# Optimization experiments

Hardware: AMD Instinct MI355X
Metric: run time of the kernel (lower is better)

## Reference

```python
import jax, jax.numpy as jnp
import numpy as np

S = 4          # num species networks (H,C,N,O)
E = 8          # ensemble size
D = 384        # AEV dim
H1, H2, H3 = 160, 128, 96
N_ATOMS = 40000
ALPHA = 0.1    # CELU alpha used by torchani


def _celu(x):
    return jax.nn.celu(x, alpha=ALPHA)


def setup_inputs() -> dict:
    key = jax.random.key(0)
    ks = jax.random.split(key, 12)
    species = jax.random.randint(ks[0], (1, N_ATOMS), 0, S, dtype=jnp.int64)
    aev = jax.random.normal(ks[1], (1, N_ATOMS, D), dtype=jnp.float32)
    def w(k, shape, fan_in):
        return jax.random.normal(k, shape, dtype=jnp.float32) * (1.0 / np.sqrt(fan_in))
    W1 = w(ks[2], (S, E, D, H1), D)
    b1 = jnp.zeros((S, E, 1, H1), jnp.float32)
    W2 = w(ks[3], (S, E, H1, H2), H1)
    b2 = jnp.zeros((S, E, 1, H2), jnp.float32)
    W3 = w(ks[4], (S, E, H2, H3), H2)
    b3 = jnp.zeros((S, E, 1, H3), jnp.float32)
    W4 = w(ks[5], (S, E, H3, 1), H3)
    b4 = jnp.zeros((S, E, 1, 1), jnp.float32)
    return {"species": species, "aev": aev,
            "W1": W1, "b1": b1, "W2": W2, "b2": b2,
            "W3": W3, "b3": b3, "W4": W4, "b4": b4}


def reference(species, aev, W1, b1, W2, b2, W3, b3, W4, b4):
    sp = species.reshape(-1)                  # [N]
    x = aev.reshape(-1, aev.shape[-1])        # [N, D]
    # BmmNetwork per species: expand input over ensemble, baddbmm + CELU layers
    h = _celu(jnp.einsum('nd,sedo->seno', x, W1) + b1)     # [S,E,N,H1]
    h = _celu(jnp.einsum('send,sedo->seno', h, W2) + b2)   # [S,E,N,H2]
    h = _celu(jnp.einsum('send,sedo->seno', h, W3) + b3)   # [S,E,N,H3]
    h = jnp.einsum('send,sedo->seno', h, W4) + b4          # [S,E,N,1]
    per_atom = h.mean(axis=1)[..., 0]                      # [S,N] ensemble mean
    # select each atom's own species network output (gather/scatter of original)
    atom_e = per_atom[sp, jnp.arange(sp.shape[0])]         # [N]
    energy = jnp.sum(atom_e).reshape(1, 1)
    return energy
```

## Files before the change

kernel.cpp:

```cpp
#include <hip/hip_runtime.h>

typedef _Float16 half8 __attribute__((ext_vector_type(8)));
typedef float f32x16 __attribute__((ext_vector_type(16)));

#define NATOMS 40000
#define D_AEV  384

constexpr int S_NUM = 4, E_NUM = 8;
constexpr int H1W = 160, H2W = 128, H3W = 96;
constexpr float ALPHA = 0.1f;
constexpr int HBLK = (NATOMS + 255) / 256;
constexpr int TMAX = NATOMS / 128 + S_NUM + 1;
constexpr int GRID = 2 * TMAX;

constexpr size_t OFF_CNT    = 0;
constexpr size_t OFF_BC     = 256;
constexpr size_t OFF_BOFF   = OFF_BC + (size_t)HBLK * S_NUM * 4;
constexpr size_t OFF_BUCKET = (OFF_BOFF + (size_t)HBLK * S_NUM * 4 + 255) & ~(size_t)255;
constexpr size_t OFF_PART   = OFF_BUCKET + (size_t)S_NUM * NATOMS * 4;
constexpr size_t OFF_WT1    = (OFF_PART + (size_t)GRID * 4 + 255) & ~(size_t)255;
constexpr size_t OFF_WT2    = OFF_WT1 + (size_t)S_NUM * E_NUM * H1W * D_AEV * 2;
constexpr size_t OFF_WT3    = OFF_WT2 + (size_t)S_NUM * E_NUM * H2W * H1W * 2;


__device__ __forceinline__ void gload_lds16(const _Float16* g, _Float16* l) {
    __builtin_amdgcn_global_load_lds((const __attribute__((address_space(1))) void*)g,
                                     (__attribute__((address_space(3))) void*)l, 16, 0, 0);
}

#define VMW(n) asm volatile("s_waitcnt vmcnt(" #n ")" ::: "memory")
#define BARR() do { asm volatile("" ::: "memory"); __builtin_amdgcn_s_barrier(); \
                    asm volatile("" ::: "memory"); } while (0)

__device__ __forceinline__ float celu_f(float x) {
    return x > 0.f ? x : fmaf(ALPHA, __expf(x * (1.f / ALPHA)), -ALPHA);
}

__device__ __forceinline__ unsigned pk2(float a, float b) {
    auto p = __builtin_amdgcn_cvt_pkrtz(a, b);
    unsigned u; __builtin_memcpy(&u, &p, 4); return u;
}

template <int NL>
__device__ __forceinline__ void stage(const _Float16* we, const int* vo, int c0, _Float16* buf) {
#pragma unroll
    for (int it = 0; it < NL; ++it)
        gload_lds16(we + vo[it] + c0, buf + ((size_t)threadIdx.x + it * 256) * 8);
}

template <int OUTW, int KS16, int NFT>
__device__ __forceinline__ void consume32(const _Float16* buf, const half8* bf,
                                          f32x16* acc, int l31, int lhi) {
    __builtin_amdgcn_s_setprio(1);
#pragma unroll
    for (int t = 0; t < KS16; ++t) {
        half8 b = bf[t];
#pragma unroll
        for (int f = 0; f < NFT; ++f) {
            half8 a = *(const half8*)&buf[(((2 * t + lhi) * OUTW) + f * 32 + l31) * 8];
            acc[f] = __builtin_amdgcn_mfma_f32_32x32x16_f16(a, b, acc[f], 0, 0, 0);
        }
    }
    __builtin_amdgcn_s_setprio(0);
}

template <int NFT>
__device__ __forceinline__ void epilogue(const f32x16* acc, const float* LB, int boff,
                                         int lhi, half8* out) {
#pragma unroll
    for (int f = 0; f < NFT; ++f) {
        float val[16];
#pragma unroll
        for (int rb = 0; rb < 4; ++rb) {
            float4 bb = *(const float4*)&LB[boff + f * 32 + rb * 8 + lhi * 4];
#pragma unroll
            for (int j = 0; j < 4; ++j)
                val[rb * 4 + j] = celu_f(acc[f][rb * 4 + j] + ((const float*)&bb)[j]);
        }
        unsigned wrd[8], xw[8];
#pragma unroll
        for (int i = 0; i < 8; ++i) wrd[i] = pk2(val[2 * i], val[2 * i + 1]);
#pragma unroll
        for (int i = 0; i < 8; ++i) xw[i] = __shfl_xor(wrd[i], 32);
        unsigned f0[4], f1[4];
#pragma unroll
        for (int i = 0; i < 2; ++i) {
            f0[i]     = lhi ? xw[2 + i]  : wrd[i];
            f0[2 + i] = lhi ? wrd[2 + i] : xw[i];
            f1[i]     = lhi ? xw[6 + i]  : wrd[4 + i];
            f1[2 + i] = lhi ? wrd[6 + i] : xw[4 + i];
        }
        __builtin_memcpy(&out[2 * f], f0, 16);
        __builtin_memcpy(&out[2 * f + 1], f1, 16);
    }
}


__global__ void hist_kernel(const int* __restrict__ species, int* __restrict__ bc) {
    __shared__ int h[S_NUM];
    int t = threadIdx.x;
    if (t < S_NUM) h[t] = 0;
    __syncthreads();
    int i = blockIdx.x * 256 + t;
    if (i < NATOMS) atomicAdd(&h[species[i]], 1);
    __syncthreads();
    if (t < S_NUM) bc[blockIdx.x * S_NUM + t] = h[t];
}

__global__ void scan_kernel(const int* __restrict__ bc, int* __restrict__ boff,
                            int* __restrict__ counts) {
    int w = threadIdx.x >> 6;
    int l = threadIdx.x & 63;
    int run = 0;
    for (int r = 0; r < (HBLK + 63) / 64; ++r) {
        int b = r * 64 + l;
        int v = (b < HBLK) ? bc[b * S_NUM + w] : 0;
        int x = v;
#pragma unroll
        for (int d = 1; d < 64; d <<= 1) { int y = __shfl_up(x, d); if (l >= d) x += y; }
        if (b < HBLK) boff[b * S_NUM + w] = run + x - v;
        run += __shfl(x, 63);
    }
    if (l == 0) counts[w] = run;
}

__global__ void scatter_kernel(const int* __restrict__ species, const int* __restrict__ boff,
                               int* __restrict__ bucket) {
    __shared__ int h[S_NUM];
    int t = threadIdx.x;
    if (t < S_NUM) h[t] = 0;
    __syncthreads();
    int i = blockIdx.x * 256 + t;
    if (i < NATOMS) {
        int sp = species[i];
        int r = atomicAdd(&h[sp], 1);
        bucket[sp * NATOMS + boff[blockIdx.x * S_NUM + sp] + r] = i;
    }
}

__global__ void transpose_all(const float* __restrict__ W1, const float* __restrict__ W2,
                              const float* __restrict__ W3, _Float16* __restrict__ wt1,
                              _Float16* __restrict__ wt2, _Float16* __restrict__ wt3) {
    __shared__ float t[32][33];
    int z = blockIdx.z;
    int m = z & 31;
    const float* src; _Float16* dst; int R, C;
    if (z < 32)      { src = W1; dst = wt1; R = D_AEV; C = H1W; }
    else if (z < 64) { src = W2; dst = wt2; R = H1W;  C = H2W; }
    else             { src = W3; dst = wt3; R = H2W;  C = H3W; }
    int c0 = blockIdx.x * 32, r0 = blockIdx.y * 32;
    if (c0 >= C || r0 >= R) return;
    src += (size_t)m * R * C;
    dst += (size_t)m * R * C;
    int tx = threadIdx.x, ty = threadIdx.y;
#pragma unroll
    for (int j = 0; j < 32; j += 8)
        t[ty + j][tx] = src[(size_t)(r0 + ty + j) * C + c0 + tx];
    __syncthreads();
#pragma unroll
    for (int j = 0; j < 32; j += 8)
        dst[(size_t)(c0 + ty + j) * R + r0 + tx] = (_Float16)t[tx][ty + j];
}


__global__ void __launch_bounds__(256, 2)
mlp_main(const int* __restrict__ counts, const int* __restrict__ bucket,
         const float* __restrict__ aev,
         const _Float16* __restrict__ wt1, const _Float16* __restrict__ wt2,
         const _Float16* __restrict__ wt3,
         const float* __restrict__ b1, const float* __restrict__ b2,
         const float* __restrict__ b3,
         const float* __restrict__ w4,
         float* __restrict__ partials) {
    __shared__ __align__(16) _Float16 WB[3][8 * H1W * 8];
    __shared__ __align__(16) float Lbias[4 * 480];
    __shared__ float part[4];

    const int bid = blockIdx.x;
    const int eb = bid & 1;
    const int t = bid >> 1;
    const int tid = threadIdx.x;

    int cnt0 = counts[0], cnt1 = counts[1], cnt2 = counts[2], cnt3 = counts[3];
    int n0 = (cnt0 + 127) >> 7, n1 = (cnt1 + 127) >> 7, n2 = (cnt2 + 127) >> 7;
    int n3 = (cnt3 + 127) >> 7;
    int s, t0, cnt;
    if (t < n0)                { s = 0; t0 = t; cnt = cnt0; }
    else if (t < n0 + n1)      { s = 1; t0 = t - n0; cnt = cnt1; }
    else if (t < n0 + n1 + n2) { s = 2; t0 = t - n0 - n1; cnt = cnt2; }
    else if (t < n0 + n1 + n2 + n3) { s = 3; t0 = t - n0 - n1 - n2; cnt = cnt3; }
    else { if (tid == 0) partials[bid] = 0.f; return; }
    const int base = t0 * 128;

    const int l = tid & 63, w = tid >> 6;
    const int l31 = l & 31, lhi = l >> 5;
    _Float16* B0 = WB[0]; _Float16* B1 = WB[1]; _Float16* B2 = WB[2];

    for (int u = tid; u < 4 * 480; u += 256) {
        int el = u / 480, o = u % 480;
        int se = s * E_NUM + eb * 4 + el;
        float v;
        if (o < 160)      v = b1[se * H1W + o];
        else if (o < 288) v = b2[se * H2W + (o - 160)];
        else if (o < 384) v = b3[se * H3W + (o - 288)];
        else              v = w4[se * H3W + (o - 384)];
        Lbias[u] = v;
    }
    __syncthreads();

    int aidx = bucket[s * NATOMS + min(base + w * 32 + l31, cnt - 1)];
    const float* xr = aev + (size_t)aidx * D_AEV + lhi * 8;
    half8 xa[24];
#pragma unroll
    for (int kk = 0; kk < 24; ++kk) {
        float4 f0 = *(const float4*)(xr + kk * 16);
        float4 f1 = *(const float4*)(xr + kk * 16 + 4);
        half8 h;
        h[0] = (_Float16)f0.x; h[1] = (_Float16)f0.y; h[2] = (_Float16)f0.z; h[3] = (_Float16)f0.w;
        h[4] = (_Float16)f1.x; h[5] = (_Float16)f1.y; h[6] = (_Float16)f1.z; h[7] = (_Float16)f1.w;
        xa[kk] = h;
    }
    VMW(0);

    int vo1[5], vo2[4], vo3[3];
#pragma unroll
    for (int it = 0; it < 5; ++it) { int u = tid + it * 256; vo1[it] = (u % H1W) * D_AEV + (u / H1W) * 8; }
#pragma unroll
    for (int it = 0; it < 4; ++it) { int u = tid + it * 256; vo2[it] = (u & 127) * H1W + (u >> 7) * 8; }
#pragma unroll
    for (int it = 0; it < 3; ++it) { int u = tid + it * 256; vo3[it] = (u % H3W) * H2W + (u / H3W) * 8; }

    float eacc = 0.f;
    const int se0 = s * E_NUM + eb * 4;

    {
        const _Float16* w1e0 = wt1 + (size_t)se0 * (H1W * D_AEV);
        stage<5>(w1e0, vo1, 0, B0);
        stage<5>(w1e0, vo1, 64, B1);
    }

#pragma unroll 1
    for (int el = 0; el < 4; ++el) {
        const int se = se0 + el;
        const _Float16* w1e = wt1 + (size_t)se * (H1W * D_AEV);
        const _Float16* w2e = wt2 + (size_t)se * (H2W * H1W);
        const _Float16* w3e = wt3 + (size_t)se * (H3W * H2W);
        const _Float16* w1n = wt1 + (size_t)(se + (el < 3 ? 1 : 0)) * (H1W * D_AEV);
        const float* LB = Lbias + el * 480;

        f32x16 c1a[5], c2a[4], c3a[3];
#pragma unroll
        for (int f = 0; f < 5; ++f) c1a[f] = (f32x16)(0.f);
#pragma unroll
        for (int f = 0; f < 4; ++f) c2a[f] = (f32x16)(0.f);
#pragma unroll
        for (int f = 0; f < 3; ++f) c3a[f] = (f32x16)(0.f);
        half8 h1f[10], h2f[8];

        stage<5>(w1e, vo1, 128, B2); VMW(10); BARR();
        consume32<H1W, 4, 5>(B0, &xa[0], c1a, l31, lhi); BARR();
        stage<5>(w1e, vo1, 192, B0); VMW(10); BARR();
        consume32<H1W, 4, 5>(B1, &xa[4], c1a, l31, lhi); BARR();
        stage<5>(w1e, vo1, 256, B1); VMW(10); BARR();
        consume32<H1W, 4, 5>(B2, &xa[8], c1a, l31, lhi); BARR();
        stage<5>(w1e, vo1, 320, B2); VMW(10); BARR();
        consume32<H1W, 4, 5>(B0, &xa[12], c1a, l31, lhi); BARR();
        stage<4>(w2e, vo2, 0, B0);   VMW(9);  BARR();
        consume32<H1W, 4, 5>(B1, &xa[16], c1a, l31, lhi); BARR();
        stage<2>(w2e, vo2, 64, B1);  VMW(6);  BARR();
        consume32<H1W, 4, 5>(B2, &xa[20], c1a, l31, lhi); BARR();

        epilogue<5>(c1a, LB, 0, lhi, h1f);

        stage<2>(w2e, vo2, 96, B2);  VMW(4);  BARR();
        consume32<H2W, 4, 4>(B0, &h1f[0], c2a, l31, lhi); BARR();
        stage<2>(w2e, vo2, 128, B0); VMW(4);  BARR();
        consume32<H2W, 2, 4>(B1, &h1f[4], c2a, l31, lhi); BARR();
        stage<3>(w3e, vo3, 0, B1);   VMW(5);  BARR();
        consume32<H2W, 2, 4>(B2, &h1f[6], c2a, l31, lhi); BARR();
        stage<3>(w3e, vo3, 64, B2);  VMW(6);  BARR();
        consume32<H2W, 2, 4>(B0, &h1f[8], c2a, l31, lhi); BARR();

        epilogue<4>(c2a, LB, 160, lhi, h2f);

        if (el < 3) { stage<5>(w1n, vo1, 0, B0); VMW(8); } else { VMW(3); }
        BARR();
        consume32<H3W, 4, 3>(B1, &h2f[0], c3a, l31, lhi); BARR();
        if (el < 3) { stage<5>(w1n, vo1, 64, B1); VMW(10); } else { VMW(0); }
        BARR();
        consume32<H3W, 4, 3>(B2, &h2f[4], c3a, l31, lhi); BARR();

        {
            float pe = 0.f;
#pragma unroll
            for (int f = 0; f < 3; ++f) {
#pragma unroll
                for (int rb = 0; rb < 4; ++rb) {
                    float4 bb = *(const float4*)&LB[288 + f * 32 + rb * 8 + lhi * 4];
                    float4 ww = *(const float4*)&LB[384 + f * 32 + rb * 8 + lhi * 4];
#pragma unroll
                    for (int j = 0; j < 4; ++j)
                        pe += celu_f(c3a[f][rb * 4 + j] + ((const float*)&bb)[j]) * ((const float*)&ww)[j];
                }
            }
            pe += __shfl_xor(pe, 32);
            eacc += pe;
        }
    }

    float v = (lhi == 0 && (base + w * 32 + l31) < cnt) ? eacc : 0.f;
#pragma unroll
    for (int m = 1; m < 64; m <<= 1) v += __shfl_xor(v, m);
    if (l == 0) part[w] = v;
    __syncthreads();
    if (tid == 0) partials[bid] = part[0] + part[1] + part[2] + part[3];
}


__global__ void finalize_kernel(const float* __restrict__ partials, const int* __restrict__ counts,
                                const float* __restrict__ b4, float* __restrict__ out) {
    __shared__ float wsum[4];
    float s = 0.f;
    for (int i = threadIdx.x; i < GRID; i += 256) s += partials[i];
#pragma unroll
    for (int m = 1; m < 64; m <<= 1) s += __shfl_xor(s, m);
    if ((threadIdx.x & 63) == 0) wsum[threadIdx.x >> 6] = s;
    __syncthreads();
    if (threadIdx.x == 0) {
        float tot = wsum[0] + wsum[1] + wsum[2] + wsum[3];
        float bt = 0.f;
        for (int sp = 0; sp < S_NUM; ++sp) {
            float bs = 0.f;
            for (int e = 0; e < E_NUM; ++e) bs += b4[sp * E_NUM + e];
            bt += (float)counts[sp] * bs;
        }
        out[0] = (tot + bt) * 0.125f;
    }
}


extern "C" void kernel_launch(void* const* d_in, const int* in_sizes, int n_in,
                              void* d_out, int out_size, void* d_ws, size_t ws_size,
                              hipStream_t stream) {
    const int*   species = (const int*)d_in[0];
    const float* aev = (const float*)d_in[1];
    const float* W1 = (const float*)d_in[2];
    const float* b1 = (const float*)d_in[3];
    const float* W2 = (const float*)d_in[4];
    const float* b2 = (const float*)d_in[5];
    const float* W3 = (const float*)d_in[6];
    const float* b3 = (const float*)d_in[7];
    const float* W4 = (const float*)d_in[8];
    const float* b4 = (const float*)d_in[9];
    float* out = (float*)d_out;

    char* ws = (char*)d_ws;
    int* counts = (int*)(ws + OFF_CNT);
    int* bc     = (int*)(ws + OFF_BC);
    int* boff   = (int*)(ws + OFF_BOFF);
    int* bucket = (int*)(ws + OFF_BUCKET);
    float* partials = (float*)(ws + OFF_PART);
    _Float16* wt1 = (_Float16*)(ws + OFF_WT1);
    _Float16* wt2 = (_Float16*)(ws + OFF_WT2);
    _Float16* wt3 = (_Float16*)(ws + OFF_WT3);

    hist_kernel<<<HBLK, 256, 0, stream>>>(species, bc);
    scan_kernel<<<1, 256, 0, stream>>>(bc, boff, counts);
    scatter_kernel<<<HBLK, 256, 0, stream>>>(species, boff, bucket);
    transpose_all<<<dim3(5, 12, 96), dim3(32, 8), 0, stream>>>(W1, W2, W3, wt1, wt2, wt3);

    mlp_main<<<GRID, 256, 0, stream>>>(
        counts, bucket, aev, wt1, wt2, wt3, b1, b2, b3, W4, partials);

    finalize_kernel<<<1, 256, 0, stream>>>(partials, counts, b4, out);
}
```

Before: 252.1 us.

## Persistent MLP kernel over per-ensemble work items with pre-sorted fp16 AEV

A new kernel gathers AEV rows into species-sorted, padded fp16 storage in a k-chunk-major layout. The MLP kernel becomes persistent with 512 blocks, each looping over (tile, ensemble-member) items. The first-layer weight staging and the activation loads for the next item are prefetched during the current item's last layer, and the biases are double-buffered in LDS through async loads. This aims to remove the per-block AEV gather and conversion prologue and the pipeline bubbles between blocks. The cost is an extra pass writing and reading the fp16 AEV copy, and activations are now reloaded for each of the 8 ensemble members instead of held in registers across 4.

```diff
diff --git a/kernel.cpp b/kernel.cpp
--- a/kernel.cpp
+++ b/kernel.cpp
@@ -10,17 +10,19 @@
 constexpr int H1W = 160, H2W = 128, H3W = 96;
 constexpr float ALPHA = 0.1f;
 constexpr int HBLK = (NATOMS + 255) / 256;
-constexpr int TMAX = NATOMS / 128 + S_NUM + 1;
-constexpr int GRID = 2 * TMAX;
+constexpr int NA2C = 40576;
+constexpr int NPB  = 512;
 
 constexpr size_t OFF_CNT    = 0;
 constexpr size_t OFF_BC     = 256;
 constexpr size_t OFF_BOFF   = OFF_BC + (size_t)HBLK * S_NUM * 4;
 constexpr size_t OFF_BUCKET = (OFF_BOFF + (size_t)HBLK * S_NUM * 4 + 255) & ~(size_t)255;
 constexpr size_t OFF_PART   = OFF_BUCKET + (size_t)S_NUM * NATOMS * 4;
-constexpr size_t OFF_WT1    = (OFF_PART + (size_t)GRID * 4 + 255) & ~(size_t)255;
+constexpr size_t OFF_WT1    = (OFF_PART + (size_t)NPB * 4 + 255) & ~(size_t)255;
 constexpr size_t OFF_WT2    = OFF_WT1 + (size_t)S_NUM * E_NUM * H1W * D_AEV * 2;
 constexpr size_t OFF_WT3    = OFF_WT2 + (size_t)S_NUM * E_NUM * H2W * H1W * 2;
+constexpr size_t OFF_AEVS   = (OFF_WT3 + (size_t)S_NUM * E_NUM * H3W * H2W * 2 + 255) & ~(size_t)255;
+constexpr size_t OFF_BIASP  = OFF_AEVS + (size_t)48 * NA2C * 8 * 2;
 
 
 __device__ __forceinline__ void gload_lds16(const _Float16* g, _Float16* l) {
@@ -138,11 +140,57 @@
     }
 }
 
+__global__ void cvt_sort_kernel(const float* __restrict__ aev, const int* __restrict__ bucket,
+                                const int* __restrict__ counts, _Float16* __restrict__ aevs) {
+    int a2 = blockIdx.x * 256 + threadIdx.x;
+    int g = blockIdx.y;
+    if (a2 >= NA2C) return;
+    int c0 = counts[0], c1 = counts[1], c2 = counts[2], c3 = counts[3];
+    int m0 = ((c0 + 127) >> 7) << 7;
+    int m1 = m0 + (((c1 + 127) >> 7) << 7);
+    int m2 = m1 + (((c2 + 127) >> 7) << 7);
+    int m3 = m2 + (((c3 + 127) >> 7) << 7);
+    if (a2 >= m3) return;
+    int s, P, cnt;
+    if (a2 < m0)      { s = 0; P = 0;  cnt = c0; }
+    else if (a2 < m1) { s = 1; P = m0; cnt = c1; }
+    else if (a2 < m2) { s = 2; P = m1; cnt = c2; }
+    else              { s = 3; P = m2; cnt = c3; }
+    int local = a2 - P;
+    half8 h = (half8)(_Float16)0.f;
+    if (local < cnt) {
+        int aidx = bucket[s * NATOMS + local];
+        const float* r = aev + (size_t)aidx * D_AEV + g * 8;
+        float4 f0 = *(const float4*)r;
+        float4 f1 = *(const float4*)(r + 4);
+        h[0] = (_Float16)f0.x; h[1] = (_Float16)f0.y; h[2] = (_Float16)f0.z; h[3] = (_Float16)f0.w;
+        h[4] = (_Float16)f1.x; h[5] = (_Float16)f1.y; h[6] = (_Float16)f1.z; h[7] = (_Float16)f1.w;
+    }
+    *(half8*)&aevs[((size_t)g * NA2C + a2) * 8] = h;
+}
+
 __global__ void transpose_all(const float* __restrict__ W1, const float* __restrict__ W2,
-                              const float* __restrict__ W3, _Float16* __restrict__ wt1,
-                              _Float16* __restrict__ wt2, _Float16* __restrict__ wt3) {
+                              const float* __restrict__ W3,
+                              const float* __restrict__ b1, const float* __restrict__ b2,
+                              const float* __restrict__ b3, const float* __restrict__ w4,
+                              _Float16* __restrict__ wt1, _Float16* __restrict__ wt2,
+                              _Float16* __restrict__ wt3, float* __restrict__ biasp) {
+    int z = blockIdx.z;
+    if (z == 96) {
+        if (blockIdx.x || blockIdx.y) return;
+        int tid = threadIdx.y * 32 + threadIdx.x;
+        for (int u = tid; u < 32 * 480; u += 256) {
+            int se = u / 480, o = u % 480;
+            float v;
+            if (o < 160)      v = b1[se * H1W + o];
+            else if (o < 288) v = b2[se * H2W + (o - 160)];
+            else if (o < 384) v = b3[se * H3W + (o - 288)];
+            else              v = w4[se * H3W + (o - 384)];
+            biasp[u] = v;
+        }
+        return;
+    }
     __shared__ float t[32][33];
-    int z = blockIdx.z;
     int m = z & 31;
     const float* src; _Float16* dst; int R, C;
     if (z < 32)      { src = W1; dst = wt1; R = D_AEV; C = H1W; }
@@ -163,90 +211,91 @@
 }
 
 
+struct Item {
+    const _Float16* w1; const _Float16* w2; const _Float16* w3;
+    const float* bp;
+    const _Float16* xb;
+    int vlim;
+    int a2lane;
+};
+
+#define XLOAD(dst, xb, c) do { \
+    dst[0] = *(const half8*)((xb) + ((size_t)((c) * 8 + 0 + lhi) * NA2C) * 8); \
+    dst[1] = *(const half8*)((xb) + ((size_t)((c) * 8 + 2 + lhi) * NA2C) * 8); \
+    dst[2] = *(const half8*)((xb) + ((size_t)((c) * 8 + 4 + lhi) * NA2C) * 8); \
+    dst[3] = *(const half8*)((xb) + ((size_t)((c) * 8 + 6 + lhi) * NA2C) * 8); } while (0)
+
 __global__ void __launch_bounds__(256, 2)
-mlp_main(const int* __restrict__ counts, const int* __restrict__ bucket,
-         const float* __restrict__ aev,
+mlp_main(const int* __restrict__ counts, const _Float16* __restrict__ aevs,
          const _Float16* __restrict__ wt1, const _Float16* __restrict__ wt2,
-         const _Float16* __restrict__ wt3,
-         const float* __restrict__ b1, const float* __restrict__ b2,
-         const float* __restrict__ b3,
-         const float* __restrict__ w4,
+         const _Float16* __restrict__ wt3, const float* __restrict__ biasp,
          float* __restrict__ partials) {
     __shared__ __align__(16) _Float16 WB[3][8 * H1W * 8];
-    __shared__ __align__(16) float Lbias[4 * 480];
+    __shared__ __align__(16) float biasL[2][1024];
     __shared__ float part[4];
 
     const int bid = blockIdx.x;
-    const int eb = bid & 1;
-    const int t = bid >> 1;
     const int tid = threadIdx.x;
-
-    int cnt0 = counts[0], cnt1 = counts[1], cnt2 = counts[2], cnt3 = counts[3];
-    int n0 = (cnt0 + 127) >> 7, n1 = (cnt1 + 127) >> 7, n2 = (cnt2 + 127) >> 7;
-    int n3 = (cnt3 + 127) >> 7;
-    int s, t0, cnt;
-    if (t < n0)                { s = 0; t0 = t; cnt = cnt0; }
-    else if (t < n0 + n1)      { s = 1; t0 = t - n0; cnt = cnt1; }
-    else if (t < n0 + n1 + n2) { s = 2; t0 = t - n0 - n1; cnt = cnt2; }
-    else if (t < n0 + n1 + n2 + n3) { s = 3; t0 = t - n0 - n1 - n2; cnt = cnt3; }
-    else { if (tid == 0) partials[bid] = 0.f; return; }
-    const int base = t0 * 128;
-
     const int l = tid & 63, w = tid >> 6;
     const int l31 = l & 31, lhi = l >> 5;
     _Float16* B0 = WB[0]; _Float16* B1 = WB[1]; _Float16* B2 = WB[2];
 
-    for (int u = tid; u < 4 * 480; u += 256) {
-        int el = u / 480, o = u % 480;
-        int se = s * E_NUM + eb * 4 + el;
-        float v;
-        if (o < 160)      v = b1[se * H1W + o];
-        else if (o < 288) v = b2[se * H2W + (o - 160)];
-        else if (o < 384) v = b3[se * H3W + (o - 288)];
-        else              v = w4[se * H3W + (o - 384)];
-        Lbias[u] = v;
-    }
-    __syncthreads();
-
-    int aidx = bucket[s * NATOMS + min(base + w * 32 + l31, cnt - 1)];
-    const float* xr = aev + (size_t)aidx * D_AEV + lhi * 8;
-    half8 xa[24];
-#pragma unroll
-    for (int kk = 0; kk < 24; ++kk) {
-        float4 f0 = *(const float4*)(xr + kk * 16);
-        float4 f1 = *(const float4*)(xr + kk * 16 + 4);
-        half8 h;
-        h[0] = (_Float16)f0.x; h[1] = (_Float16)f0.y; h[2] = (_Float16)f0.z; h[3] = (_Float16)f0.w;
-        h[4] = (_Float16)f1.x; h[5] = (_Float16)f1.y; h[6] = (_Float16)f1.z; h[7] = (_Float16)f1.w;
-        xa[kk] = h;
-    }
-    VMW(0);
-
-    int vo1[5], vo2[4], vo3[3];
+    const int c0 = counts[0], c1 = counts[1], c2 = counts[2], c3 = counts[3];
+    const int n0 = (c0 + 127) >> 7, n1 = (c1 + 127) >> 7, n2 = (c2 + 127) >> 7, n3 = (c3 + 127) >> 7;
+    const int m0 = n0, m1 = n0 + n1, m2 = m1 + n2, NT = m2 + n3;
+    const int NITEMS = NT * 8;
+    if (bid >= NITEMS) { if (tid == 0) partials[bid] = 0.f; return; }
+
+    int vo1[5], vo2a[4], vo3a[3], vo3b[2];
 #pragma unroll
     for (int it = 0; it < 5; ++it) { int u = tid + it * 256; vo1[it] = (u % H1W) * D_AEV + (u / H1W) * 8; }
 #pragma unroll
-    for (int it = 0; it < 4; ++it) { int u = tid + it * 256; vo2[it] = (u & 127) * H1W + (u >> 7) * 8; }
-#pragma unroll
-    for (int it = 0; it < 3; ++it) { int u = tid + it * 256; vo3[it] = (u % H3W) * H2W + (u / H3W) * 8; }
-
-    float eacc = 0.f;
-    const int se0 = s * E_NUM + eb * 4;
-
-    {
-        const _Float16* w1e0 = wt1 + (size_t)se0 * (H1W * D_AEV);
-        stage<5>(w1e0, vo1, 0, B0);
-        stage<5>(w1e0, vo1, 64, B1);
-    }
+    for (int it = 0; it < 4; ++it) { int u = tid + it * 256; vo2a[it] = (u & 127) * H1W + (u >> 7) * 8; }
+#pragma unroll
+    for (int it = 0; it < 3; ++it) { int u = tid + it * 256; vo3a[it] = (u % H3W) * H2W + (u / H3W) * 8; }
+#pragma unroll
+    for (int it = 0; it < 2; ++it) { int u = tid + it * 256; vo3b[it] = (u < 384) ? (u % H3W) * H2W + (u / H3W) * 8 : 0; }
+    const int biasoff = (tid < 120 ? tid : 119) * 8;
+
+    auto decode = [&](int it) {
+        Item I;
+        int e = it & 7, t = it >> 3;
+        int s, P, cnt;
+        if (t < m0)      { s = 0; P = 0;        cnt = c0; }
+        else if (t < m1) { s = 1; P = m0 * 128; cnt = c1; }
+        else if (t < m2) { s = 2; P = m1 * 128; cnt = c2; }
+        else             { s = 3; P = m2 * 128; cnt = c3; }
+        int se = s * E_NUM + e;
+        I.w1 = wt1 + (size_t)se * (H1W * D_AEV);
+        I.w2 = wt2 + (size_t)se * (H2W * H1W);
+        I.w3 = wt3 + (size_t)se * (H3W * H2W);
+        I.bp = biasp + se * 480;
+        I.a2lane = t * 128 + w * 32 + l31;
+        I.xb = aevs + (size_t)I.a2lane * 8;
+        I.vlim = P + cnt;
+        return I;
+    };
+
+    float wacc = 0.f;
+    half8 xv0[4], xv1[4], xv2[4];
+    half8 h1f[10], h2f[8];
+
+    Item cur = decode(bid);
+    stage<5>(cur.w1, vo1, 0, B0);
+    XLOAD(xv0, cur.xb, 0);
+    gload_lds16((const _Float16*)cur.bp + biasoff, (_Float16*)&biasL[0][0] + tid * 8);
+    stage<5>(cur.w1, vo1, 64, B1);
+    XLOAD(xv1, cur.xb, 1);
+
+    int ip = 0;
 
 #pragma unroll 1
-    for (int el = 0; el < 4; ++el) {
-        const int se = se0 + el;
-        const _Float16* w1e = wt1 + (size_t)se * (H1W * D_AEV);
-        const _Float16* w2e = wt2 + (size_t)se * (H2W * H1W);
-        const _Float16* w3e = wt3 + (size_t)se * (H3W * H2W);
-        const _Float16* w1n = wt1 + (size_t)(se + (el < 3 ? 1 : 0)) * (H1W * D_AEV);
-        const float* LB = Lbias + el * 480;
+    for (int it = bid; it < NITEMS; it += NPB) {
+        int itn = it + NPB;
+        bool hn = itn < NITEMS;
+        Item nxt = hn ? decode(itn) : cur;
+        const float* LB = &biasL[ip][0];
+        float* LBn = &biasL[ip ^ 1][0];
 
         f32x16 c1a[5], c2a[4], c3a[3];
 #pragma unroll
@@ -255,40 +304,44 @@
         for (int f = 0; f < 4; ++f) c2a[f] = (f32x16)(0.f);
 #pragma unroll
         for (int f = 0; f < 3; ++f) c3a[f] = (f32x16)(0.f);
-        half8 h1f[10], h2f[8];
-
-        stage<5>(w1e, vo1, 128, B2); VMW(10); BARR();
-        consume32<H1W, 4, 5>(B0, &xa[0], c1a, l31, lhi); BARR();
-        stage<5>(w1e, vo1, 192, B0); VMW(10); BARR();
-        consume32<H1W, 4, 5>(B1, &xa[4], c1a, l31, lhi); BARR();
-        stage<5>(w1e, vo1, 256, B1); VMW(10); BARR();
-        consume32<H1W, 4, 5>(B2, &xa[8], c1a, l31, lhi); BARR();
-        stage<5>(w1e, vo1, 320, B2); VMW(10); BARR();
-        consume32<H1W, 4, 5>(B0, &xa[12], c1a, l31, lhi); BARR();
-        stage<4>(w2e, vo2, 0, B0);   VMW(9);  BARR();
-        consume32<H1W, 4, 5>(B1, &xa[16], c1a, l31, lhi); BARR();
-        stage<2>(w2e, vo2, 64, B1);  VMW(6);  BARR();
-        consume32<H1W, 4, 5>(B2, &xa[20], c1a, l31, lhi); BARR();
+
+        stage<5>(cur.w1, vo1, 128, B2); XLOAD(xv2, cur.xb, 2);
+        VMW(18); BARR(); consume32<H1W, 4, 5>(B0, xv0, c1a, l31, lhi); BARR();
+        stage<5>(cur.w1, vo1, 192, B0); XLOAD(xv0, cur.xb, 3);
+        VMW(18); BARR(); consume32<H1W, 4, 5>(B1, xv1, c1a, l31, lhi); BARR();
+        stage<5>(cur.w1, vo1, 256, B1); XLOAD(xv1, cur.xb, 4);
+        VMW(18); BARR(); consume32<H1W, 4, 5>(B2, xv2, c1a, l31, lhi); BARR();
+        stage<5>(cur.w1, vo1, 320, B2); XLOAD(xv2, cur.xb, 5);
+        VMW(18); BARR(); consume32<H1W, 4, 5>(B0, xv0, c1a, l31, lhi); BARR();
+        stage<4>(cur.w2, vo2a, 0, B0);
+        VMW(13); BARR(); consume32<H1W, 4, 5>(B1, xv1, c1a, l31, lhi); BARR();
+        stage<4>(cur.w2, vo2a, 64, B1);
+        VMW(8); BARR(); consume32<H1W, 4, 5>(B2, xv2, c1a, l31, lhi); BARR();
 
         epilogue<5>(c1a, LB, 0, lhi, h1f);
 
-        stage<2>(w2e, vo2, 96, B2);  VMW(4);  BARR();
-        consume32<H2W, 4, 4>(B0, &h1f[0], c2a, l31, lhi); BARR();
-        stage<2>(w2e, vo2, 128, B0); VMW(4);  BARR();
-        consume32<H2W, 2, 4>(B1, &h1f[4], c2a, l31, lhi); BARR();
-        stage<3>(w3e, vo3, 0, B1);   VMW(5);  BARR();
-        consume32<H2W, 2, 4>(B2, &h1f[6], c2a, l31, lhi); BARR();
-        stage<3>(w3e, vo3, 64, B2);  VMW(6);  BARR();
-        consume32<H2W, 2, 4>(B0, &h1f[8], c2a, l31, lhi); BARR();
+        stage<2>(cur.w2, vo2a, 128, B2);
+        VMW(6); BARR(); consume32<H2W, 4, 4>(B0, &h1f[0], c2a, l31, lhi); BARR();
+        stage<3>(cur.w3, vo3a, 0, B0);
+        VMW(5); BARR(); consume32<H2W, 4, 4>(B1, &h1f[4], c2a, l31, lhi); BARR();
+        stage<2>(cur.w3, vo3b, 64, B1);
+        VMW(5); BARR(); consume32<H2W, 2, 4>(B2, &h1f[8], c2a, l31, lhi); BARR();
 
         epilogue<4>(c2a, LB, 160, lhi, h2f);
 
-        if (el < 3) { stage<5>(w1n, vo1, 0, B0); VMW(8); } else { VMW(3); }
-        BARR();
-        consume32<H3W, 4, 3>(B1, &h2f[0], c3a, l31, lhi); BARR();
-        if (el < 3) { stage<5>(w1n, vo1, 64, B1); VMW(10); } else { VMW(0); }
-        BARR();
-        consume32<H3W, 4, 3>(B2, &h2f[4], c3a, l31, lhi); BARR();
+        stage<2>(cur.w3, vo3b, 96, B2);
+        VMW(4); BARR(); consume32<H3W, 4, 3>(B0, &h2f[0], c3a, l31, lhi); BARR();
+        if (hn) {
+            stage<5>(nxt.w1, vo1, 0, B0); XLOAD(xv0, nxt.xb, 0);
+            gload_lds16((const _Float16*)nxt.bp + biasoff, (_Float16*)LBn + tid * 8);
+            VMW(12);
+        } else { VMW(2); }
+        BARR(); consume32<H3W, 2, 3>(B1, &h2f[4], c3a, l31, lhi); BARR();
+        if (hn) {
+            stage<5>(nxt.w1, vo1, 64, B1); XLOAD(xv1, nxt.xb, 1);
+            VMW(19);
+        } else { VMW(0); }
+        BARR(); consume32<H3W, 2, 3>(B2, &h2f[6], c3a, l31, lhi); BARR();
 
         {
             float pe = 0.f;
@@ -304,14 +357,16 @@
                 }
             }
             pe += __shfl_xor(pe, 32);
-            eacc += pe;
-        }
-    }
-
-    float v = (lhi == 0 && (base + w * 32 + l31) < cnt) ? eacc : 0.f;
-#pragma unroll
-    for (int m = 1; m < 64; m <<= 1) v += __shfl_xor(v, m);
-    if (l == 0) part[w] = v;
+            if (lhi == 0 && cur.a2lane < cur.vlim) wacc += pe;
+        }
+
+        cur = nxt;
+        ip ^= 1;
+    }
+
+#pragma unroll
+    for (int m = 1; m < 64; m <<= 1) wacc += __shfl_xor(wacc, m);
+    if (l == 0) part[w] = wacc;
     __syncthreads();
     if (tid == 0) partials[bid] = part[0] + part[1] + part[2] + part[3];
 }
@@ -321,7 +376,7 @@
                                 const float* __restrict__ b4, float* __restrict__ out) {
     __shared__ float wsum[4];
     float s = 0.f;
-    for (int i = threadIdx.x; i < GRID; i += 256) s += partials[i];
+    for (int i = threadIdx.x; i < NPB; i += 256) s += partials[i];
 #pragma unroll
     for (int m = 1; m < 64; m <<= 1) s += __shfl_xor(s, m);
     if ((threadIdx.x & 63) == 0) wsum[threadIdx.x >> 6] = s;
@@ -363,14 +418,17 @@
     _Float16* wt1 = (_Float16*)(ws + OFF_WT1);
     _Float16* wt2 = (_Float16*)(ws + OFF_WT2);
     _Float16* wt3 = (_Float16*)(ws + OFF_WT3);
+    _Float16* aevs = (_Float16*)(ws + OFF_AEVS);
+    float* biasp = (float*)(ws + OFF_BIASP);
 
     hist_kernel<<<HBLK, 256, 0, stream>>>(species, bc);
     scan_kernel<<<1, 256, 0, stream>>>(bc, boff, counts);
     scatter_kernel<<<HBLK, 256, 0, stream>>>(species, boff, bucket);
-    transpose_all<<<dim3(5, 12, 96), dim3(32, 8), 0, stream>>>(W1, W2, W3, wt1, wt2, wt3);
-
-    mlp_main<<<GRID, 256, 0, stream>>>(
-        counts, bucket, aev, wt1, wt2, wt3, b1, b2, b3, W4, partials);
+    transpose_all<<<dim3(5, 12, 97), dim3(32, 8), 0, stream>>>(W1, W2, W3, b1, b2, b3, W4,
+                                                               wt1, wt2, wt3, biasp);
+    cvt_sort_kernel<<<dim3((NA2C + 255) / 256, 48), 256, 0, stream>>>(aev, bucket, counts, aevs);
+
+    mlp_main<<<NPB, 256, 0, stream>>>(counts, aevs, wt1, wt2, wt3, biasp, partials);
 
     finalize_kernel<<<1, 256, 0, stream>>>(partials, counts, b4, out);
 }
```

Measured after the change: 264.7 us. 1.05x slower.
